# Kernel tuning notes

Measured on AMD Instinct MI355X. Metric: run time of the kernel, lower is better.

Reference implementation:

```python
import jax, jax.numpy as jnp
import numpy as np

N = 50000      # nodes
E = 800000     # edges (before self-loops)
F_IN = 128     # num_features
H = 4          # heads
C = 64         # hidden_channels
HC = H * C     # 256
NEG_SLOPE = 0.2


def setup_inputs() -> dict:
    key = jax.random.key(0)
    ks = jax.random.split(key, 20)
    x = jax.random.normal(ks[0], (N, F_IN), dtype=jnp.float32)
    edge_index = jax.random.randint(ks[1], (2, E), 0, N, dtype=jnp.int32)
    s = 0.05
    inp = {"x": x, "edge_index": edge_index}
    dims_in = [F_IN, HC, HC, HC]
    for l in range(4):
        kW, ka, kb = jax.random.split(ks[2 + l], 3)
        inp[f"W{l+1}"] = jax.random.normal(kW, (dims_in[l], HC), dtype=jnp.float32) * s
        inp[f"a_src{l+1}"] = jax.random.normal(ka, (H, C), dtype=jnp.float32) * s
        inp[f"a_dst{l+1}"] = jax.random.normal(kb, (H, C), dtype=jnp.float32) * s
        inp[f"b{l+1}"] = jnp.zeros((HC,), dtype=jnp.float32)
    return inp


def gat_conv(x, src, dst, W, a_src, a_dst, b):
    # x: [N, F_in] -> h: [N, H, C]
    h = (x @ W).reshape(N, H, C)
    es = jnp.sum(h * a_src, axis=-1)  # [N, H] per-node source logits
    ed = jnp.sum(h * a_dst, axis=-1)  # [N, H]
    e = jax.nn.leaky_relu(es[src] + ed[dst], NEG_SLOPE)  # [Etot, H]
    m = jax.ops.segment_max(e, dst, num_segments=N)      # per-dst max
    m = jnp.where(jnp.isfinite(m), m, 0.0)
    ex = jnp.exp(e - m[dst])
    denom = jax.ops.segment_sum(ex, dst, num_segments=N)
    alpha = ex / (denom[dst] + 1e-16)                     # edge softmax
    out = jax.ops.segment_sum(alpha[:, :, None] * h[src], dst, num_segments=N)
    return out.reshape(N, HC) + b


def reference(x, edge_index,
              W1, a_src1, a_dst1, b1,
              W2, a_src2, a_dst2, b2,
              W3, a_src3, a_dst3, b3,
              W4, a_src4, a_dst4, b4):
    loop = jnp.arange(N, dtype=edge_index.dtype)
    src = jnp.concatenate([edge_index[0], loop])  # add self-loops (PyG default)
    dst = jnp.concatenate([edge_index[1], loop])
    x1 = jax.nn.relu(gat_conv(x, src, dst, W1, a_src1, a_dst1, b1))
    x2 = jax.nn.relu(gat_conv(x1, src, dst, W2, a_src2, a_dst2, b2))
    x3 = jax.nn.relu(gat_conv(x2 + x1, src, dst, W3, a_src3, a_dst3, b3))
    x4 = jax.nn.relu(gat_conv(x2 + x3, src, dst, W4, a_src4, a_dst4, b4))
    # NOTE: source code calls conv4 again (not conv5) -- reproduced faithfully
    x5 = gat_conv(x4 + x3, src, dst, W4, a_src4, a_dst4, b4)
    return x5
```

## Files before the change

### kernel.cpp

```cpp
#include <hip/hip_runtime.h>
#include <hip/hip_bf16.h>

#define N_NODES 50000
#define E_EDGES 800000
#define ETOT (E_EDGES + N_NODES)
#define HC 256
#define NHEAD 4
#define CHAN 64
#define NEG 0.2f
#define NBLK ((N_NODES + 1023) / 1024)

typedef _Float16 half8 __attribute__((ext_vector_type(8)));
typedef _Float16 half4v __attribute__((ext_vector_type(4)));
typedef float float4v __attribute__((ext_vector_type(4)));


__global__ void count_kernel(const int* __restrict__ ei, int* __restrict__ counts) {
    int i = blockIdx.x * blockDim.x + threadIdx.x;
    if (i >= ETOT) return;
    int dst = (i < E_EDGES) ? ei[E_EDGES + i] : (i - E_EDGES);
    atomicAdd(&counts[dst], 1);
}

__global__ __launch_bounds__(256) void blocksum_kernel(const int* __restrict__ counts,
                                                       int* __restrict__ blocksums) {
    __shared__ int s[4];
    int b = blockIdx.x, tid = threadIdx.x;
    int base = b * 1024;
    int sum = 0;
    #pragma unroll
    for (int r = 0; r < 4; ++r) {
        int idx = base + r * 256 + tid;
        sum += (idx < N_NODES) ? counts[idx] : 0;
    }
    #pragma unroll
    for (int m = 1; m < 64; m <<= 1) sum += __shfl_xor(sum, m, 64);
    if ((tid & 63) == 0) s[tid >> 6] = sum;
    __syncthreads();
    if (tid == 0) blocksums[b] = s[0] + s[1] + s[2] + s[3];
}

__global__ __launch_bounds__(64) void blockscan_kernel(int* __restrict__ blocksums) {
    int tid = threadIdx.x;
    int v = (tid < NBLK) ? blocksums[tid] : 0;
    #pragma unroll
    for (int off = 1; off < 64; off <<= 1) {
        int t = __shfl_up(v, off, 64);
        if (tid >= off) v += t;
    }
    if (tid < NBLK) blocksums[tid] = v;
}

__global__ __launch_bounds__(1024) void scatter_scan_kernel(const int* __restrict__ counts,
                                                            const int* __restrict__ blocksums,
                                                            int* __restrict__ offsets,
                                                            int* __restrict__ cursor) {
    __shared__ int s[1024];
    int b = blockIdx.x, tid = threadIdx.x;
    int idx = b * 1024 + tid;
    int v = (idx < N_NODES) ? counts[idx] : 0;
    s[tid] = v;
    __syncthreads();
    for (int off = 1; off < 1024; off <<= 1) {
        int t = (tid >= off) ? s[tid - off] : 0;
        __syncthreads();
        s[tid] += t;
        __syncthreads();
    }
    int excl = s[tid] - v + (b > 0 ? blocksums[b - 1] : 0);
    if (idx < N_NODES) { offsets[idx] = excl; cursor[idx] = excl; }
    if (idx == N_NODES - 1) offsets[N_NODES] = excl + v;
}

__global__ void fill_kernel(const int* __restrict__ ei, int* __restrict__ cursor,
                            int* __restrict__ csr_src) {
    int i = blockIdx.x * blockDim.x + threadIdx.x;
    if (i >= ETOT) return;
    int src, dst;
    if (i < E_EDGES) { src = ei[i]; dst = ei[E_EDGES + i]; }
    else             { src = i - E_EDGES; dst = src; }
    int pos = atomicAdd(&cursor[dst], 1);
    csr_src[pos] = src;
}


__global__ void wsplit_kernel(const float* __restrict__ W, _Float16* __restrict__ Wth,
                              _Float16* __restrict__ Wtl, int K) {
    int id = blockIdx.x * 256 + threadIdx.x;
    if (id >= K * 256) return;
    int n = id & 255, k = id >> 8;
    float w = W[(size_t)k * 256 + n];
    _Float16 h = (_Float16)w;
    _Float16 l = (_Float16)(w - (float)h);
    Wth[(size_t)n * K + k] = h;
    Wtl[(size_t)n * K + k] = l;
}


#define LDK 40

__global__ __launch_bounds__(256) void gemm_mfma_kernel(
        const float* __restrict__ A1, const float* __restrict__ A2,
        const _Float16* __restrict__ Wth, const _Float16* __restrict__ Wtl,
        _Float16* __restrict__ H16, int M, int K) {
    __shared__ _Float16 Ah[128][LDK];
    __shared__ _Float16 Al[128][LDK];
    __shared__ _Float16 Bh[128][LDK];
    __shared__ _Float16 Bl[128][LDK];

    int tid = threadIdx.x;
    int m0 = blockIdx.x * 128;
    int n0 = blockIdx.y * 128;
    int w = tid >> 6, lane = tid & 63;
    int rm = (w & 1) * 64, rn = (w >> 1) * 64;
    int fr = lane & 15;
    int fk = (lane >> 4) * 8;

    int ar = tid >> 3;
    int ak = (tid & 7) * 4;
    int wr = tid >> 2;
    int wk = (tid & 3) * 8;

    float4v acc[4][4];
    #pragma unroll
    for (int i = 0; i < 4; ++i)
        #pragma unroll
        for (int j = 0; j < 4; ++j)
            acc[i][j] = (float4v){0.f, 0.f, 0.f, 0.f};

    for (int k0 = 0; k0 < K; k0 += 32) {
        __syncthreads();
        #pragma unroll
        for (int g = 0; g < 4; ++g) {
            int r = g * 32 + ar;
            int row = m0 + r;
            float4 v = make_float4(0.f, 0.f, 0.f, 0.f);
            if (row < M) {
                v = *(const float4*)(A1 + (size_t)row * K + k0 + ak);
                if (A2) {
                    float4 u = *(const float4*)(A2 + (size_t)row * K + k0 + ak);
                    v.x += u.x; v.y += u.y; v.z += u.z; v.w += u.w;
                }
            }
            half4v hv = {(_Float16)v.x, (_Float16)v.y, (_Float16)v.z, (_Float16)v.w};
            half4v lv = {(_Float16)(v.x - (float)hv[0]), (_Float16)(v.y - (float)hv[1]),
                         (_Float16)(v.z - (float)hv[2]), (_Float16)(v.w - (float)hv[3])};
            *(half4v*)&Ah[r][ak] = hv;
            *(half4v*)&Al[r][ak] = lv;
        }
        #pragma unroll
        for (int g = 0; g < 2; ++g) {
            int r = g * 64 + wr;
            const _Float16* ph = Wth + (size_t)(n0 + r) * K + k0 + wk;
            const _Float16* pl = Wtl + (size_t)(n0 + r) * K + k0 + wk;
            *(half8*)&Bh[r][wk] = *(const half8*)ph;
            *(half8*)&Bl[r][wk] = *(const half8*)pl;
        }
        __syncthreads();
        half8 afh[4], afl[4], bfh[4], bfl[4];
        #pragma unroll
        for (int t = 0; t < 4; ++t) {
            afh[t] = *(const half8*)&Ah[rm + t * 16 + fr][fk];
            afl[t] = *(const half8*)&Al[rm + t * 16 + fr][fk];
            bfh[t] = *(const half8*)&Bh[rn + t * 16 + fr][fk];
            bfl[t] = *(const half8*)&Bl[rn + t * 16 + fr][fk];
        }
        #pragma unroll
        for (int tm = 0; tm < 4; ++tm)
            #pragma unroll
            for (int tn = 0; tn < 4; ++tn) {
                float4v c = acc[tm][tn];
                c = __builtin_amdgcn_mfma_f32_16x16x32_f16(afl[tm], bfh[tn], c, 0, 0, 0);
                c = __builtin_amdgcn_mfma_f32_16x16x32_f16(afh[tm], bfl[tn], c, 0, 0, 0);
                c = __builtin_amdgcn_mfma_f32_16x16x32_f16(afh[tm], bfh[tn], c, 0, 0, 0);
                acc[tm][tn] = c;
            }
    }
    #pragma unroll
    for (int tm = 0; tm < 4; ++tm) {
        int rbase = m0 + rm + tm * 16 + (lane >> 4) * 4;
        #pragma unroll
        for (int i = 0; i < 4; ++i) {
            int row = rbase + i;
            if (row < M) {
                #pragma unroll
                for (int tn = 0; tn < 4; ++tn)
                    H16[(size_t)row * HC + n0 + rn + tn * 16 + fr] = (_Float16)acc[tm][tn][i];
            }
        }
    }
}


__global__ __launch_bounds__(256) void esed_kernel(const _Float16* __restrict__ H16,
                                                   const float* __restrict__ a_src,
                                                   const float* __restrict__ a_dst,
                                                   float* __restrict__ es, float* __restrict__ ed) {
    int tid = threadIdx.x;
    int lane = tid & 63;
    int node = blockIdx.x * 4 + (tid >> 6);
    int head = lane >> 4;
    int cc = (lane & 15) * 4;
    half4v hv = *(const half4v*)(H16 + (size_t)node * HC + lane * 4);
    float4 h4 = make_float4((float)hv[0], (float)hv[1], (float)hv[2], (float)hv[3]);
    float4 as = *(const float4*)(a_src + head * CHAN + cc);
    float4 ad = *(const float4*)(a_dst + head * CHAN + cc);
    float ps = h4.x * as.x + h4.y * as.y + h4.z * as.z + h4.w * as.w;
    float pd = h4.x * ad.x + h4.y * ad.y + h4.z * ad.z + h4.w * ad.w;
    #pragma unroll
    for (int m = 1; m < 16; m <<= 1) {
        ps += __shfl_xor(ps, m, 64);
        pd += __shfl_xor(pd, m, 64);
    }
    if ((lane & 15) == 0) {
        es[node * NHEAD + head] = ps;
        ed[node * NHEAD + head] = pd;
    }
}


__global__ __launch_bounds__(256) void gat_aggregate_kernel(
        const _Float16* __restrict__ H16, const float* __restrict__ es, const float* __restrict__ ed,
        const int* __restrict__ offsets, const int* __restrict__ csr_src,
        const float* __restrict__ bias, float* __restrict__ out, int do_relu) {
    __shared__ float alpha_lds[4][256];
    int tid = threadIdx.x;
    int w = tid >> 6, lane = tid & 63;
    int n = blockIdx.x * 4 + w;
    int off = offsets[n];
    int deg = offsets[n + 1] - off;
    int head = lane >> 4;
    float4 edv = *(const float4*)(ed + (size_t)n * 4);
    float4 acc0 = make_float4(0.f, 0.f, 0.f, 0.f);
    float4 acc1 = make_float4(0.f, 0.f, 0.f, 0.f);

    if (deg <= 64) {
        int sreg = 0;
        float4 e4 = make_float4(-1e30f, -1e30f, -1e30f, -1e30f);
        if (lane < deg) {
            sreg = csr_src[off + lane];
            float4 esv = *(const float4*)(es + (size_t)sreg * 4);
            e4.x = esv.x + edv.x; e4.y = esv.y + edv.y;
            e4.z = esv.z + edv.z; e4.w = esv.w + edv.w;
            e4.x = (e4.x > 0.f) ? e4.x : NEG * e4.x;
            e4.y = (e4.y > 0.f) ? e4.y : NEG * e4.y;
            e4.z = (e4.z > 0.f) ? e4.z : NEG * e4.z;
            e4.w = (e4.w > 0.f) ? e4.w : NEG * e4.w;
        }
        float4 m4 = e4;
        #pragma unroll
        for (int msk = 1; msk < 64; msk <<= 1) {
            m4.x = fmaxf(m4.x, __shfl_xor(m4.x, msk, 64));
            m4.y = fmaxf(m4.y, __shfl_xor(m4.y, msk, 64));
            m4.z = fmaxf(m4.z, __shfl_xor(m4.z, msk, 64));
            m4.w = fmaxf(m4.w, __shfl_xor(m4.w, msk, 64));
        }
        float4 ex4 = make_float4(0.f, 0.f, 0.f, 0.f);
        if (lane < deg) {
            ex4.x = __expf(e4.x - m4.x); ex4.y = __expf(e4.y - m4.y);
            ex4.z = __expf(e4.z - m4.z); ex4.w = __expf(e4.w - m4.w);
        }
        float4 l4 = ex4;
        #pragma unroll
        for (int msk = 1; msk < 64; msk <<= 1) {
            l4.x += __shfl_xor(l4.x, msk, 64);
            l4.y += __shfl_xor(l4.y, msk, 64);
            l4.z += __shfl_xor(l4.z, msk, 64);
            l4.w += __shfl_xor(l4.w, msk, 64);
        }
        float4 a4;
        a4.x = ex4.x / (l4.x + 1e-16f);
        a4.y = ex4.y / (l4.y + 1e-16f);
        a4.z = ex4.z / (l4.z + 1e-16f);
        a4.w = ex4.w / (l4.w + 1e-16f);
        *(float4*)&alpha_lds[w][lane * 4] = a4;

        int j = 0;
        #pragma unroll 2
        for (; j + 4 <= deg; j += 4) {
            int s0 = __shfl(sreg, j,     64);
            int s1 = __shfl(sreg, j + 1, 64);
            int s2 = __shfl(sreg, j + 2, 64);
            int s3 = __shfl(sreg, j + 3, 64);
            float al0 = alpha_lds[w][(j    ) * 4 + head];
            float al1 = alpha_lds[w][(j + 1) * 4 + head];
            float al2 = alpha_lds[w][(j + 2) * 4 + head];
            float al3 = alpha_lds[w][(j + 3) * 4 + head];
            half4v h0 = *(const half4v*)(H16 + (size_t)s0 * HC + lane * 4);
            half4v h1 = *(const half4v*)(H16 + (size_t)s1 * HC + lane * 4);
            half4v h2 = *(const half4v*)(H16 + (size_t)s2 * HC + lane * 4);
            half4v h3 = *(const half4v*)(H16 + (size_t)s3 * HC + lane * 4);
            acc0.x += al0 * (float)h0[0]; acc0.y += al0 * (float)h0[1];
            acc0.z += al0 * (float)h0[2]; acc0.w += al0 * (float)h0[3];
            acc1.x += al1 * (float)h1[0]; acc1.y += al1 * (float)h1[1];
            acc1.z += al1 * (float)h1[2]; acc1.w += al1 * (float)h1[3];
            acc0.x += al2 * (float)h2[0]; acc0.y += al2 * (float)h2[1];
            acc0.z += al2 * (float)h2[2]; acc0.w += al2 * (float)h2[3];
            acc1.x += al3 * (float)h3[0]; acc1.y += al3 * (float)h3[1];
            acc1.z += al3 * (float)h3[2]; acc1.w += al3 * (float)h3[3];
        }
        for (; j < deg; ++j) {
            int s0 = __shfl(sreg, j, 64);
            float al0 = alpha_lds[w][j * 4 + head];
            half4v h0 = *(const half4v*)(H16 + (size_t)s0 * HC + lane * 4);
            acc0.x += al0 * (float)h0[0]; acc0.y += al0 * (float)h0[1];
            acc0.z += al0 * (float)h0[2]; acc0.w += al0 * (float)h0[3];
        }
    } else {
        float m[4] = {-1e30f, -1e30f, -1e30f, -1e30f};
        float l[4] = {0.f, 0.f, 0.f, 0.f};
        for (int base = 0; base < deg; base += 64) {
            int j = base + lane;
            if (j < deg) {
                int s = csr_src[off + j];
                float4 esv = *(const float4*)(es + (size_t)s * 4);
                float e[4] = {esv.x + edv.x, esv.y + edv.y, esv.z + edv.z, esv.w + edv.w};
                #pragma unroll
                for (int h = 0; h < 4; ++h) {
                    e[h] = (e[h] > 0.f) ? e[h] : NEG * e[h];
                    float M2 = fmaxf(m[h], e[h]);
                    l[h] = l[h] * __expf(m[h] - M2) + __expf(e[h] - M2);
                    m[h] = M2;
                }
            }
        }
        #pragma unroll
        for (int msk = 1; msk < 64; msk <<= 1) {
            #pragma unroll
            for (int h = 0; h < 4; ++h) {
                float mo = __shfl_xor(m[h], msk, 64);
                float lo = __shfl_xor(l[h], msk, 64);
                float M2 = fmaxf(m[h], mo);
                l[h] = l[h] * __expf(m[h] - M2) + lo * __expf(mo - M2);
                m[h] = M2;
            }
        }
        float fm = m[head];
        float fr = 1.f / (l[head] + 1e-16f);
        float edh = ((const float*)&edv)[head];
        for (int j = 0; j < deg; ++j) {
            int s = csr_src[off + j];
            float e = es[(size_t)s * 4 + head] + edh;
            e = (e > 0.f) ? e : NEG * e;
            float alpha = __expf(e - fm) * fr;
            half4v h0 = *(const half4v*)(H16 + (size_t)s * HC + lane * 4);
            acc0.x += alpha * (float)h0[0]; acc0.y += alpha * (float)h0[1];
            acc0.z += alpha * (float)h0[2]; acc0.w += alpha * (float)h0[3];
        }
    }

    float4 b4 = *(const float4*)(bias + lane * 4);
    float4 o;
    o.x = acc0.x + acc1.x + b4.x; o.y = acc0.y + acc1.y + b4.y;
    o.z = acc0.z + acc1.z + b4.z; o.w = acc0.w + acc1.w + b4.w;
    if (do_relu) {
        o.x = fmaxf(o.x, 0.f); o.y = fmaxf(o.y, 0.f);
        o.z = fmaxf(o.z, 0.f); o.w = fmaxf(o.w, 0.f);
    }
    *(float4*)(out + (size_t)n * HC + lane * 4) = o;
}


extern "C" void kernel_launch(void* const* d_in, const int* in_sizes, int n_in,
                              void* d_out, int out_size, void* d_ws, size_t ws_size,
                              hipStream_t stream) {
    const float* x  = (const float*)d_in[0];
    const int*   ei = (const int*)d_in[1];
    const float *W[5], *Asrc[5], *Adst[5], *Bs[5];
    for (int l = 0; l < 4; ++l) {
        W[l]    = (const float*)d_in[2 + l * 4];
        Asrc[l] = (const float*)d_in[3 + l * 4];
        Adst[l] = (const float*)d_in[4 + l * 4];
        Bs[l]   = (const float*)d_in[5 + l * 4];
    }
    W[4] = W[3]; Asrc[4] = Asrc[3]; Adst[4] = Adst[3]; Bs[4] = Bs[3];

    char* ws = (char*)d_ws;
    size_t off = 0;
    auto alloc = [&](size_t bytes) -> void* {
        void* p = ws + off;
        off += (bytes + 255) & ~(size_t)255;
        return p;
    };
    _Float16* h16  = (_Float16*)alloc((size_t)N_NODES * HC * 2);
    float* xa      = (float*)alloc((size_t)N_NODES * HC * 4);
    float* xb      = (float*)alloc((size_t)N_NODES * HC * 4);
    float* xc      = (float*)alloc((size_t)N_NODES * HC * 4);
    float* es      = (float*)alloc((size_t)N_NODES * 4 * 4);
    float* ed      = (float*)alloc((size_t)N_NODES * 4 * 4);
    int*   counts  = (int*)alloc((size_t)N_NODES * 4);
    int*   offsets = (int*)alloc((size_t)(N_NODES + 1) * 4);
    int*   cursor  = (int*)alloc((size_t)N_NODES * 4);
    int*   csr_src = (int*)alloc((size_t)ETOT * 4);
    int*   blocksums = (int*)alloc((size_t)NBLK * 4);
    _Float16 *Wth[5], *Wtl[5];
    int Ks[4] = {128, 256, 256, 256};
    for (int l = 0; l < 4; ++l) {
        Wth[l] = (_Float16*)alloc((size_t)256 * Ks[l] * 2);
        Wtl[l] = (_Float16*)alloc((size_t)256 * Ks[l] * 2);
    }
    Wth[4] = Wth[3]; Wtl[4] = Wtl[3];

    hipMemsetAsync(counts, 0, (size_t)N_NODES * 4, stream);
    count_kernel<<<(ETOT + 255) / 256, 256, 0, stream>>>(ei, counts);
    blocksum_kernel<<<NBLK, 256, 0, stream>>>(counts, blocksums);
    blockscan_kernel<<<1, 64, 0, stream>>>(blocksums);
    scatter_scan_kernel<<<NBLK, 1024, 0, stream>>>(counts, blocksums, offsets, cursor);
    fill_kernel<<<(ETOT + 255) / 256, 256, 0, stream>>>(ei, cursor, csr_src);
    for (int l = 0; l < 4; ++l)
        wsplit_kernel<<<(Ks[l] * 256 + 255) / 256, 256, 0, stream>>>(W[l], Wth[l], Wtl[l], Ks[l]);

    auto layer = [&](const float* in1, const float* in2, int K, int l, float* outp, int relu) {
        dim3 g((N_NODES + 127) / 128, 2);
        gemm_mfma_kernel<<<g, 256, 0, stream>>>(in1, in2, Wth[l], Wtl[l], h16, N_NODES, K);
        esed_kernel<<<N_NODES / 4, 256, 0, stream>>>(h16, Asrc[l], Adst[l], es, ed);
        gat_aggregate_kernel<<<N_NODES / 4, 256, 0, stream>>>(h16, es, ed, offsets, csr_src,
                                                              Bs[l], outp, relu);
    };

    float* out = (float*)d_out;
    layer(x,  nullptr, 128, 0, xa, 1);
    layer(xa, nullptr, 256, 1, xb, 1);
    layer(xb, xa,      256, 2, xc, 1);
    layer(xb, xc,      256, 3, xa, 1);
    layer(xa, xc,      256, 4, out, 0);
}
```

Measured before the change: 889.7 us.

## Retile GEMM to full-width 64x256 blocks and widen aggregate gathers to half8

The GEMM now gives each block 64 rows and all 256 output columns, so the fp32 activation rows (plus the optional residual add) are read and split into fp16 hi/lo once instead of once per column half. The B tile grows to hold the whole weight slice, which increases LDS use per block. In the low-degree aggregate path, each half-wave handles alternate edges with 16-byte half8 loads per lane, and the two halves are combined with a cross-lane shuffle before a single half-wave writes the output. This doubles bytes per gather instruction and halves loop trips, at the cost of idling half the wave during the store.

```diff
diff --git a/kernel.cpp b/kernel.cpp
--- a/kernel.cpp
+++ b/kernel.cpp
@@ -103,16 +103,15 @@
         const float* __restrict__ A1, const float* __restrict__ A2,
         const _Float16* __restrict__ Wth, const _Float16* __restrict__ Wtl,
         _Float16* __restrict__ H16, int M, int K) {
-    __shared__ _Float16 Ah[128][LDK];
-    __shared__ _Float16 Al[128][LDK];
-    __shared__ _Float16 Bh[128][LDK];
-    __shared__ _Float16 Bl[128][LDK];
+    __shared__ _Float16 Ah[64][LDK];
+    __shared__ _Float16 Al[64][LDK];
+    __shared__ _Float16 Bh[256][LDK];
+    __shared__ _Float16 Bl[256][LDK];
 
     int tid = threadIdx.x;
-    int m0 = blockIdx.x * 128;
-    int n0 = blockIdx.y * 128;
+    int m0 = blockIdx.x * 64;
     int w = tid >> 6, lane = tid & 63;
-    int rm = (w & 1) * 64, rn = (w >> 1) * 64;
+    int rn = w * 64;
     int fr = lane & 15;
     int fk = (lane >> 4) * 8;
 
@@ -131,7 +130,7 @@
     for (int k0 = 0; k0 < K; k0 += 32) {
         __syncthreads();
         #pragma unroll
-        for (int g = 0; g < 4; ++g) {
+        for (int g = 0; g < 2; ++g) {
             int r = g * 32 + ar;
             int row = m0 + r;
             float4 v = make_float4(0.f, 0.f, 0.f, 0.f);
@@ -149,19 +148,17 @@
             *(half4v*)&Al[r][ak] = lv;
         }
         #pragma unroll
-        for (int g = 0; g < 2; ++g) {
+        for (int g = 0; g < 4; ++g) {
             int r = g * 64 + wr;
-            const _Float16* ph = Wth + (size_t)(n0 + r) * K + k0 + wk;
-            const _Float16* pl = Wtl + (size_t)(n0 + r) * K + k0 + wk;
-            *(half8*)&Bh[r][wk] = *(const half8*)ph;
-            *(half8*)&Bl[r][wk] = *(const half8*)pl;
+            *(half8*)&Bh[r][wk] = *(const half8*)(Wth + (size_t)r * K + k0 + wk);
+            *(half8*)&Bl[r][wk] = *(const half8*)(Wtl + (size_t)r * K + k0 + wk);
         }
         __syncthreads();
         half8 afh[4], afl[4], bfh[4], bfl[4];
         #pragma unroll
         for (int t = 0; t < 4; ++t) {
-            afh[t] = *(const half8*)&Ah[rm + t * 16 + fr][fk];
-            afl[t] = *(const half8*)&Al[rm + t * 16 + fr][fk];
+            afh[t] = *(const half8*)&Ah[t * 16 + fr][fk];
+            afl[t] = *(const half8*)&Al[t * 16 + fr][fk];
             bfh[t] = *(const half8*)&Bh[rn + t * 16 + fr][fk];
             bfl[t] = *(const half8*)&Bl[rn + t * 16 + fr][fk];
         }
@@ -178,14 +175,14 @@
     }
     #pragma unroll
     for (int tm = 0; tm < 4; ++tm) {
-        int rbase = m0 + rm + tm * 16 + (lane >> 4) * 4;
+        int rbase = m0 + tm * 16 + (lane >> 4) * 4;
         #pragma unroll
         for (int i = 0; i < 4; ++i) {
             int row = rbase + i;
             if (row < M) {
                 #pragma unroll
                 for (int tn = 0; tn < 4; ++tn)
-                    H16[(size_t)row * HC + n0 + rn + tn * 16 + fr] = (_Float16)acc[tm][tn][i];
+                    H16[(size_t)row * HC + rn + tn * 16 + fr] = (_Float16)acc[tm][tn][i];
             }
         }
     }
@@ -229,10 +226,7 @@
     int n = blockIdx.x * 4 + w;
     int off = offsets[n];
     int deg = offsets[n + 1] - off;
-    int head = lane >> 4;
     float4 edv = *(const float4*)(ed + (size_t)n * 4);
-    float4 acc0 = make_float4(0.f, 0.f, 0.f, 0.f);
-    float4 acc1 = make_float4(0.f, 0.f, 0.f, 0.f);
 
     if (deg <= 64) {
         int sreg = 0;
@@ -275,84 +269,82 @@
         a4.w = ex4.w / (l4.w + 1e-16f);
         *(float4*)&alpha_lds[w][lane * 4] = a4;
 
-        int j = 0;
+        int hl = lane & 31, side = lane >> 5;
+        int hd = hl >> 3;
+        float av[8] = {0.f, 0.f, 0.f, 0.f, 0.f, 0.f, 0.f, 0.f};
         #pragma unroll 2
-        for (; j + 4 <= deg; j += 4) {
-            int s0 = __shfl(sreg, j,     64);
-            int s1 = __shfl(sreg, j + 1, 64);
-            int s2 = __shfl(sreg, j + 2, 64);
-            int s3 = __shfl(sreg, j + 3, 64);
-            float al0 = alpha_lds[w][(j    ) * 4 + head];
-            float al1 = alpha_lds[w][(j + 1) * 4 + head];
-            float al2 = alpha_lds[w][(j + 2) * 4 + head];
-            float al3 = alpha_lds[w][(j + 3) * 4 + head];
-            half4v h0 = *(const half4v*)(H16 + (size_t)s0 * HC + lane * 4);
-            half4v h1 = *(const half4v*)(H16 + (size_t)s1 * HC + lane * 4);
-            half4v h2 = *(const half4v*)(H16 + (size_t)s2 * HC + lane * 4);
-            half4v h3 = *(const half4v*)(H16 + (size_t)s3 * HC + lane * 4);
-            acc0.x += al0 * (float)h0[0]; acc0.y += al0 * (float)h0[1];
-            acc0.z += al0 * (float)h0[2]; acc0.w += al0 * (float)h0[3];
-            acc1.x += al1 * (float)h1[0]; acc1.y += al1 * (float)h1[1];
-            acc1.z += al1 * (float)h1[2]; acc1.w += al1 * (float)h1[3];
-            acc0.x += al2 * (float)h2[0]; acc0.y += al2 * (float)h2[1];
-            acc0.z += al2 * (float)h2[2]; acc0.w += al2 * (float)h2[3];
-            acc1.x += al3 * (float)h3[0]; acc1.y += al3 * (float)h3[1];
-            acc1.z += al3 * (float)h3[2]; acc1.w += al3 * (float)h3[3];
-        }
-        for (; j < deg; ++j) {
-            int s0 = __shfl(sreg, j, 64);
-            float al0 = alpha_lds[w][j * 4 + head];
-            half4v h0 = *(const half4v*)(H16 + (size_t)s0 * HC + lane * 4);
-            acc0.x += al0 * (float)h0[0]; acc0.y += al0 * (float)h0[1];
-            acc0.z += al0 * (float)h0[2]; acc0.w += al0 * (float)h0[3];
-        }
-    } else {
-        float m[4] = {-1e30f, -1e30f, -1e30f, -1e30f};
-        float l[4] = {0.f, 0.f, 0.f, 0.f};
-        for (int base = 0; base < deg; base += 64) {
-            int j = base + lane;
-            if (j < deg) {
-                int s = csr_src[off + j];
-                float4 esv = *(const float4*)(es + (size_t)s * 4);
-                float e[4] = {esv.x + edv.x, esv.y + edv.y, esv.z + edv.z, esv.w + edv.w};
-                #pragma unroll
-                for (int h = 0; h < 4; ++h) {
-                    e[h] = (e[h] > 0.f) ? e[h] : NEG * e[h];
-                    float M2 = fmaxf(m[h], e[h]);
-                    l[h] = l[h] * __expf(m[h] - M2) + __expf(e[h] - M2);
-                    m[h] = M2;
-                }
+        for (int j = side; j < deg; j += 2) {
+            int s = __shfl(sreg, j, 64);
+            float al = alpha_lds[w][j * 4 + hd];
+            half8 hv = *(const half8*)(H16 + (size_t)s * HC + hl * 8);
+            #pragma unroll
+            for (int c = 0; c < 8; ++c) av[c] += al * (float)hv[c];
+        }
+        #pragma unroll
+        for (int c = 0; c < 8; ++c) av[c] += __shfl_xor(av[c], 32, 64);
+        if (side == 0) {
+            float4 b0 = *(const float4*)(bias + hl * 8);
+            float4 b1 = *(const float4*)(bias + hl * 8 + 4);
+            float4 o0 = make_float4(av[0] + b0.x, av[1] + b0.y, av[2] + b0.z, av[3] + b0.w);
+            float4 o1 = make_float4(av[4] + b1.x, av[5] + b1.y, av[6] + b1.z, av[7] + b1.w);
+            if (do_relu) {
+                o0.x = fmaxf(o0.x, 0.f); o0.y = fmaxf(o0.y, 0.f);
+                o0.z = fmaxf(o0.z, 0.f); o0.w = fmaxf(o0.w, 0.f);
+                o1.x = fmaxf(o1.x, 0.f); o1.y = fmaxf(o1.y, 0.f);
+                o1.z = fmaxf(o1.z, 0.f); o1.w = fmaxf(o1.w, 0.f);
             }
-        }
-        #pragma unroll
-        for (int msk = 1; msk < 64; msk <<= 1) {
+            *(float4*)(out + (size_t)n * HC + hl * 8) = o0;
+            *(float4*)(out + (size_t)n * HC + hl * 8 + 4) = o1;
+        }
+        return;
+    }
+
+    int head = lane >> 4;
+    float4 acc0 = make_float4(0.f, 0.f, 0.f, 0.f);
+    float m[4] = {-1e30f, -1e30f, -1e30f, -1e30f};
+    float l[4] = {0.f, 0.f, 0.f, 0.f};
+    for (int base = 0; base < deg; base += 64) {
+        int j = base + lane;
+        if (j < deg) {
+            int s = csr_src[off + j];
+            float4 esv = *(const float4*)(es + (size_t)s * 4);
+            float e[4] = {esv.x + edv.x, esv.y + edv.y, esv.z + edv.z, esv.w + edv.w};
             #pragma unroll
             for (int h = 0; h < 4; ++h) {
-                float mo = __shfl_xor(m[h], msk, 64);
-                float lo = __shfl_xor(l[h], msk, 64);
-                float M2 = fmaxf(m[h], mo);
-                l[h] = l[h] * __expf(m[h] - M2) + lo * __expf(mo - M2);
+                e[h] = (e[h] > 0.f) ? e[h] : NEG * e[h];
+                float M2 = fmaxf(m[h], e[h]);
+                l[h] = l[h] * __expf(m[h] - M2) + __expf(e[h] - M2);
                 m[h] = M2;
             }
         }
-        float fm = m[head];
-        float fr = 1.f / (l[head] + 1e-16f);
-        float edh = ((const float*)&edv)[head];
-        for (int j = 0; j < deg; ++j) {
-            int s = csr_src[off + j];
-            float e = es[(size_t)s * 4 + head] + edh;
-            e = (e > 0.f) ? e : NEG * e;
-            float alpha = __expf(e - fm) * fr;
-            half4v h0 = *(const half4v*)(H16 + (size_t)s * HC + lane * 4);
-            acc0.x += alpha * (float)h0[0]; acc0.y += alpha * (float)h0[1];
-            acc0.z += alpha * (float)h0[2]; acc0.w += alpha * (float)h0[3];
-        }
-    }
-
+    }
+    #pragma unroll
+    for (int msk = 1; msk < 64; msk <<= 1) {
+        #pragma unroll
+        for (int h = 0; h < 4; ++h) {
+            float mo = __shfl_xor(m[h], msk, 64);
+            float lo = __shfl_xor(l[h], msk, 64);
+            float M2 = fmaxf(m[h], mo);
+            l[h] = l[h] * __expf(m[h] - M2) + lo * __expf(mo - M2);
+            m[h] = M2;
+        }
+    }
+    float fm = m[head];
+    float fr = 1.f / (l[head] + 1e-16f);
+    float edh = ((const float*)&edv)[head];
+    for (int j = 0; j < deg; ++j) {
+        int s = csr_src[off + j];
+        float e = es[(size_t)s * 4 + head] + edh;
+        e = (e > 0.f) ? e : NEG * e;
+        float alpha = __expf(e - fm) * fr;
+        half4v h0 = *(const half4v*)(H16 + (size_t)s * HC + lane * 4);
+        acc0.x += alpha * (float)h0[0]; acc0.y += alpha * (float)h0[1];
+        acc0.z += alpha * (float)h0[2]; acc0.w += alpha * (float)h0[3];
+    }
     float4 b4 = *(const float4*)(bias + lane * 4);
     float4 o;
-    o.x = acc0.x + acc1.x + b4.x; o.y = acc0.y + acc1.y + b4.y;
-    o.z = acc0.z + acc1.z + b4.z; o.w = acc0.w + acc1.w + b4.w;
+    o.x = acc0.x + b4.x; o.y = acc0.y + b4.y;
+    o.z = acc0.z + b4.z; o.w = acc0.w + b4.w;
     if (do_relu) {
         o.x = fmaxf(o.x, 0.f); o.y = fmaxf(o.y, 0.f);
         o.z = fmaxf(o.z, 0.f); o.w = fmaxf(o.w, 0.f);
@@ -411,8 +403,8 @@
         wsplit_kernel<<<(Ks[l] * 256 + 255) / 256, 256, 0, stream>>>(W[l], Wth[l], Wtl[l], Ks[l]);
 
     auto layer = [&](const float* in1, const float* in2, int K, int l, float* outp, int relu) {
-        dim3 g((N_NODES + 127) / 128, 2);
-        gemm_mfma_kernel<<<g, 256, 0, stream>>>(in1, in2, Wth[l], Wtl[l], h16, N_NODES, K);
+        gemm_mfma_kernel<<<(N_NODES + 63) / 64, 256, 0, stream>>>(in1, in2, Wth[l], Wtl[l],
+                                                                  h16, N_NODES, K);
         esed_kernel<<<N_NODES / 4, 256, 0, stream>>>(h16, Asrc[l], Adst[l], es, ed);
         gat_aggregate_kernel<<<N_NODES / 4, 256, 0, stream>>>(h16, es, ed, offsets, csr_src,
                                                               Bs[l], outp, relu);
```

Result: no change. 887.4 us (-0.3%).
